# Performance work log

Hardware: AMD Instinct MI355X
Metric: run time of the kernel (lower is better)

## Reference

```python
import jax, jax.numpy as jnp
from jax import lax
import numpy as np

ALPHA = 0.82
MAXITER = 10
N1_NODES = 2048
N2_NODES = 2048
K_ATTR = 64
EDGE_P = 0.004  # sparse-ish adjacency density


def setup_inputs() -> dict:
    key = jax.random.key(0)
    k1, k2, k3, k4 = jax.random.split(key, 4)
    A1 = (jax.random.uniform(k1, (N1_NODES, N1_NODES)) < EDGE_P).astype(jnp.float32)
    A1 = jnp.maximum(A1, A1.T)  # undirected 0/1 adjacency
    A2 = (jax.random.uniform(k2, (N2_NODES, N2_NODES)) < EDGE_P).astype(jnp.float32)
    A2 = jnp.maximum(A2, A2.T)
    N1 = jax.random.uniform(k3, (N1_NODES, K_ATTR), dtype=jnp.float32)
    N2 = jax.random.uniform(k4, (N2_NODES, K_ATTR), dtype=jnp.float32)
    # default prior (_get_H with path=None), normalized so sum ~= 1
    H = jnp.full((N2_NODES, N1_NODES), 1.0 / (N1_NODES * N2_NODES), dtype=jnp.float32)
    return {"A1": A1, "A2": A2, "N1": N1, "N2": N2, "H": H}


def _row_l2_normalize(N):
    nrm = jnp.sqrt(jnp.sum(N * N, axis=1, keepdims=True))
    return jnp.where(nrm > 0, N / jnp.where(nrm > 0, nrm, 1.0), 0.0)


def _final_forward(A1, A2, N1, N2, H, alpha=ALPHA, maxiter=MAXITER):
    # No edge attrs: L=1, E1=A1, E2=A2. T = 1/A^2 where A^2>0 (elementwise),
    # E <- E*T, so B = (E*A) = A*T*A.
    def masked_recip_sq(A):
        A2e = A * A
        return jnp.where(A2e > 0, 1.0 / jnp.where(A2e > 0, A2e, 1.0), 0.0)

    B1 = (A1 * masked_recip_sq(A1)) * A1  # (n1, n1)
    B2 = (A2 * masked_recip_sq(A2)) * A2  # (n2, n2)

    N1n = _row_l2_normalize(N1)  # (n1, K)
    N2n = _row_l2_normalize(N2)  # (n2, K)

    # Kronecker vectors laid out as (n1, n2) matrices (C-order == kron order):
    # N[i*n2+j] = sum_k N1[i,k]*N2[j,k]  -> N1n @ N2n.T
    Nm = N1n @ N2n.T  # (n1, n2)
    dm = (B1 @ N1n) @ (B2 @ N2n).T  # (n1, n2)
    D = Nm * dm
    DD = jnp.where(D > 0, lax.rsqrt(jnp.where(D > 0, D, 1.0)), 0.0)  # inf -> 0
    q = DD * Nm  # (n1, n2)

    # h = H.flatten('F') with H (n2,n1): as an (n1,n2) matrix this is H.T
    h = H.T  # (n1, n2)

    def step(s, _):
        # M = (q*s) reshaped (n2,n1) F-order == (q*s).T in our layout.
        # S = B2 @ M @ B1 (n2,n1); S.flatten('F') as (n1,n2) == B1.T @ (q*s) @ B2.T
        S_t = B1.T @ (q * s) @ B2.T  # (n1, n2)
        s_new = (1.0 - alpha) * h + alpha * q * S_t
        return s_new, None

    s, _ = lax.scan(step, h, None, length=maxiter)
    # original: s.reshape((n1, n2)) C-order -> exactly our layout
    return s  # (n1, n2) alignment matrix


def reference(A1, A2, N1, N2, H):
    return _final_forward(A1, A2, N1, N2, H)
```

## Files before the change

kernel.cpp:

```cpp
#include <hip/hip_runtime.h>

#define NMAT 2048
#define KATTR 64
#define CAP 128
#define NITER 10

typedef unsigned short ushort4v __attribute__((ext_vector_type(4)));

__device__ __forceinline__ unsigned short f2bf(float f) {
  unsigned u = __float_as_uint(f);
  return (unsigned short)((u + 0x7fff + ((u >> 16) & 1)) >> 16);
}
__device__ __forceinline__ float bf2f(unsigned short b) {
  return __uint_as_float((unsigned)b << 16);
}
__device__ __forceinline__ float bflo(unsigned v) {
  return __uint_as_float(v << 16);
}
__device__ __forceinline__ float bfhi(unsigned v) {
  return __uint_as_float(v & 0xffff0000u);
}
__device__ __forceinline__ int swz(int c) { return 4 * c + (((c >> 3) & 7) << 2); }

__global__ __launch_bounds__(256) void k_build(
    const float* __restrict__ A, unsigned short* __restrict__ idx,
    unsigned short* __restrict__ idxT, int* __restrict__ cnt) {
  __shared__ int lcnt;
  int r = blockIdx.x;
  if (threadIdx.x == 0) lcnt = 0;
  __syncthreads();
  const float* row = A + (size_t)r * NMAT;
  for (int c = threadIdx.x; c < NMAT; c += 256) {
    if (row[c] != 0.0f) {
      int p = atomicAdd(&lcnt, 1);
      if (p < CAP) {
        idx[r * CAP + p] = (unsigned short)c;
        if (idxT) idxT[(size_t)p * NMAT + r] = (unsigned short)c;
      }
    }
  }
  __syncthreads();
  if (threadIdx.x == 0) cnt[r] = lcnt < CAP ? lcnt : CAP;
}

__global__ __launch_bounds__(256) void k_norm(const float* __restrict__ Nin,
                                              float* __restrict__ Nout) {
  int row = blockIdx.x * 4 + (threadIdx.x >> 6);
  int lane = threadIdx.x & 63;
  float v = Nin[(size_t)row * KATTR + lane];
  float ss = v * v;
#pragma unroll
  for (int o = 32; o > 0; o >>= 1) ss += __shfl_xor(ss, o);
  float nrm = sqrtf(ss);
  Nout[(size_t)row * KATTR + lane] = (nrm > 0.f) ? v / nrm : 0.f;
}

__global__ void k_gatherN(const unsigned short* __restrict__ idx,
                          const int* __restrict__ cnt,
                          const float* __restrict__ Nn,
                          float* __restrict__ C) {
  int i = blockIdx.x;
  int lane = threadIdx.x;
  int nn = cnt[i];
  const unsigned short* ip = idx + i * CAP;
  float acc = 0.f;
  for (int t = 0; t < nn; ++t) {
    int k = ip[t];
    acc += Nn[(size_t)k * KATTR + lane];
  }
  C[(size_t)i * KATTR + lane] = acc;
}

__global__ __launch_bounds__(256) void k_transpose(const float* __restrict__ H,
                                                   float* __restrict__ Ht) {
  __shared__ float tile[64][65];
  int j0 = blockIdx.x * 64;
  int i0 = blockIdx.y * 64;
  int c = threadIdx.x & 63;
  int r0 = threadIdx.x >> 6;
  for (int r = r0; r < 64; r += 4)
    tile[r][c] = H[(size_t)(j0 + r) * NMAT + i0 + c];
  __syncthreads();
  for (int r = r0; r < 64; r += 4)
    Ht[(size_t)(i0 + r) * NMAT + j0 + c] = tile[c][r];
}

__global__ __launch_bounds__(256) void k_q(
    const float* __restrict__ N1n, const float* __restrict__ C1,
    const float* __restrict__ N2n, const float* __restrict__ C2,
    const float* __restrict__ Ht, float* __restrict__ q,
    float* __restrict__ Q2, unsigned short* __restrict__ M,
    unsigned short* __restrict__ M0base) {
  __shared__ float sA[64][68];
  __shared__ float sB[64][68];
  int i0 = blockIdx.y * 64, j0 = blockIdx.x * 64;
  int c = threadIdx.x & 63, r0 = threadIdx.x >> 6;
  int tx = threadIdx.x & 15, ty = threadIdx.x >> 4;
  const float alpha = 0.82f;

  float nmv[4][4] = {};
  float dmv[4][4] = {};

  for (int r = r0; r < 64; r += 4) {
    sA[c][r] = N1n[(size_t)(i0 + r) * KATTR + c];
    sB[c][r] = N2n[(size_t)(j0 + r) * KATTR + c];
  }
  __syncthreads();
#pragma unroll 4
  for (int k = 0; k < 64; ++k) {
    float4 a = *(const float4*)&sA[k][ty * 4];
    float4 b = *(const float4*)&sB[k][tx * 4];
    float av[4] = {a.x, a.y, a.z, a.w};
    float bv[4] = {b.x, b.y, b.z, b.w};
#pragma unroll
    for (int ii = 0; ii < 4; ++ii)
#pragma unroll
      for (int jj = 0; jj < 4; ++jj)
        nmv[ii][jj] = fmaf(av[ii], bv[jj], nmv[ii][jj]);
  }
  __syncthreads();
  for (int r = r0; r < 64; r += 4) {
    sA[c][r] = C1[(size_t)(i0 + r) * KATTR + c];
    sB[c][r] = C2[(size_t)(j0 + r) * KATTR + c];
  }
  __syncthreads();
#pragma unroll 4
  for (int k = 0; k < 64; ++k) {
    float4 a = *(const float4*)&sA[k][ty * 4];
    float4 b = *(const float4*)&sB[k][tx * 4];
    float av[4] = {a.x, a.y, a.z, a.w};
    float bv[4] = {b.x, b.y, b.z, b.w};
#pragma unroll
    for (int ii = 0; ii < 4; ++ii)
#pragma unroll
      for (int jj = 0; jj < 4; ++jj)
        dmv[ii][jj] = fmaf(av[ii], bv[jj], dmv[ii][jj]);
  }

#pragma unroll
  for (int ii = 0; ii < 4; ++ii) {
    int i = i0 + ty * 4 + ii;
    size_t base = (size_t)i * NMAT + j0 + tx * 4;
    float4 hv = *(const float4*)&Ht[base];
    float hvv[4] = {hv.x, hv.y, hv.z, hv.w};
    float qv[4], q2v[4];
    ushort4v mv, m0v;
#pragma unroll
    for (int jj = 0; jj < 4; ++jj) {
      float nmx = nmv[ii][jj];
      float D = nmx * dmv[ii][jj];
      float qq = (D > 0.f) ? nmx * rsqrtf(D) : 0.f;
      qv[jj] = qq;
      q2v[jj] = alpha * qq * qq;
      float m0 = qq * hvv[jj];
      mv[jj] = f2bf(m0);
      m0v[jj] = f2bf((1.0f - alpha) * m0);
    }
    *(float4*)&q[base] = make_float4(qv[0], qv[1], qv[2], qv[3]);
    *(float4*)&Q2[base] = make_float4(q2v[0], q2v[1], q2v[2], q2v[3]);
    *(ushort4v*)&M[base] = mv;
    *(ushort4v*)&M0base[base] = m0v;
  }
}

__global__ __launch_bounds__(1024, 8) void k_iter(
    const unsigned short* __restrict__ idx1, const int* __restrict__ cnt1,
    const unsigned short* __restrict__ idx2T, const int* __restrict__ cnt2,
    const unsigned short* __restrict__ Min, const float* __restrict__ MinF,
    const float* __restrict__ Q2, const unsigned short* __restrict__ M0base,
    const float* __restrict__ q, const float* __restrict__ Ht,
    unsigned short* __restrict__ Mout, float* __restrict__ MoutF,
    float* __restrict__ sout, int in32, int out32, int last) {
  __shared__ float lds[4 * NMAT + 32];
  int i0 = blockIdx.x * 4;
  int tid = threadIdx.x;
  int c0 = tid * 2;

  float acc[4][2];
#pragma unroll
  for (int r = 0; r < 4; ++r) {
    int nn = cnt1[i0 + r];
    const unsigned short* ip = idx1 + (i0 + r) * CAP;
    float a0 = 0.f, a1 = 0.f;
    float b0 = 0.f, b1 = 0.f;
    if (in32) {
      int t = 0;
      for (; t + 4 <= nn; t += 4) {
        uint2 pk = *(const uint2*)(ip + t);
        int k0 = pk.x & 0xffff, k1 = pk.x >> 16;
        int k2 = pk.y & 0xffff, k3 = pk.y >> 16;
        float2 v0 = *(const float2*)(MinF + (size_t)k0 * NMAT + c0);
        float2 v1 = *(const float2*)(MinF + (size_t)k1 * NMAT + c0);
        float2 v2 = *(const float2*)(MinF + (size_t)k2 * NMAT + c0);
        float2 v3 = *(const float2*)(MinF + (size_t)k3 * NMAT + c0);
        a0 += v0.x + v1.x; a1 += v0.y + v1.y;
        b0 += v2.x + v3.x; b1 += v2.y + v3.y;
      }
      for (; t < nn; ++t) {
        float2 v0 = *(const float2*)(MinF + (size_t)ip[t] * NMAT + c0);
        a0 += v0.x; a1 += v0.y;
      }
    } else {
      int t = 0;
      for (; t + 8 <= nn; t += 8) {
        uint4 pk = *(const uint4*)(ip + t);
        int k0 = pk.x & 0xffff, k1 = pk.x >> 16;
        int k2 = pk.y & 0xffff, k3 = pk.y >> 16;
        int k4 = pk.z & 0xffff, k5 = pk.z >> 16;
        int k6 = pk.w & 0xffff, k7 = pk.w >> 16;
        unsigned v0 = *(const unsigned*)(Min + (size_t)k0 * NMAT + c0);
        unsigned v1 = *(const unsigned*)(Min + (size_t)k1 * NMAT + c0);
        unsigned v2 = *(const unsigned*)(Min + (size_t)k2 * NMAT + c0);
        unsigned v3 = *(const unsigned*)(Min + (size_t)k3 * NMAT + c0);
        unsigned v4 = *(const unsigned*)(Min + (size_t)k4 * NMAT + c0);
        unsigned v5 = *(const unsigned*)(Min + (size_t)k5 * NMAT + c0);
        unsigned v6 = *(const unsigned*)(Min + (size_t)k6 * NMAT + c0);
        unsigned v7 = *(const unsigned*)(Min + (size_t)k7 * NMAT + c0);
        a0 += bflo(v0) + bflo(v1) + bflo(v2) + bflo(v3);
        a1 += bfhi(v0) + bfhi(v1) + bfhi(v2) + bfhi(v3);
        b0 += bflo(v4) + bflo(v5) + bflo(v6) + bflo(v7);
        b1 += bfhi(v4) + bfhi(v5) + bfhi(v6) + bfhi(v7);
      }
      for (; t + 4 <= nn; t += 4) {
        uint2 pk = *(const uint2*)(ip + t);
        int k0 = pk.x & 0xffff, k1 = pk.x >> 16;
        int k2 = pk.y & 0xffff, k3 = pk.y >> 16;
        unsigned v0 = *(const unsigned*)(Min + (size_t)k0 * NMAT + c0);
        unsigned v1 = *(const unsigned*)(Min + (size_t)k1 * NMAT + c0);
        unsigned v2 = *(const unsigned*)(Min + (size_t)k2 * NMAT + c0);
        unsigned v3 = *(const unsigned*)(Min + (size_t)k3 * NMAT + c0);
        a0 += bflo(v0) + bflo(v1) + bflo(v2) + bflo(v3);
        a1 += bfhi(v0) + bfhi(v1) + bfhi(v2) + bfhi(v3);
      }
      for (; t < nn; ++t) {
        unsigned v0 = *(const unsigned*)(Min + (size_t)ip[t] * NMAT + c0);
        a0 += bflo(v0); a1 += bfhi(v0);
      }
    }
    acc[r][0] = a0 + b0;
    acc[r][1] = a1 + b1;
  }
  *(float4*)&lds[swz(c0)] =
      make_float4(acc[0][0], acc[1][0], acc[2][0], acc[3][0]);
  *(float4*)&lds[swz(c0 + 1)] =
      make_float4(acc[0][1], acc[1][1], acc[2][1], acc[3][1]);
  __syncthreads();

  const float alpha = 0.82f;
  const float oma = 1.0f - alpha;
#pragma unroll
  for (int jj = 0; jj < 2; ++jj) {
    int j = jj * 1024 + tid;
    int nn = cnt2[j];
    const unsigned short* ip = idx2T + j;
    float s0 = 0.f, s1 = 0.f, s2 = 0.f, s3 = 0.f;
    float u0 = 0.f, u1 = 0.f, u2 = 0.f, u3 = 0.f;
    int t = 0;
    for (; t + 4 <= nn; t += 4) {
      int ka = ip[(size_t)t * NMAT];
      int kb = ip[(size_t)(t + 1) * NMAT];
      int kc = ip[(size_t)(t + 2) * NMAT];
      int kd = ip[(size_t)(t + 3) * NMAT];
      float4 va = *(const float4*)&lds[swz(ka)];
      float4 vb = *(const float4*)&lds[swz(kb)];
      float4 vc = *(const float4*)&lds[swz(kc)];
      float4 vd = *(const float4*)&lds[swz(kd)];
      s0 += va.x + vc.x; s1 += va.y + vc.y;
      s2 += va.z + vc.z; s3 += va.w + vc.w;
      u0 += vb.x + vd.x; u1 += vb.y + vd.y;
      u2 += vb.z + vd.z; u3 += vb.w + vd.w;
    }
    for (; t < nn; ++t) {
      int ka = ip[(size_t)t * NMAT];
      float4 va = *(const float4*)&lds[swz(ka)];
      s0 += va.x; s1 += va.y; s2 += va.z; s3 += va.w;
    }
    float sa[4] = {s0 + u0, s1 + u1, s2 + u2, s3 + u3};
    if (last) {
#pragma unroll
      for (int r = 0; r < 4; ++r) {
        size_t off = (size_t)(i0 + r) * NMAT + j;
        sout[off] = oma * Ht[off] + alpha * q[off] * sa[r];
      }
    } else if (out32) {
#pragma unroll
      for (int r = 0; r < 4; ++r) {
        size_t off = (size_t)(i0 + r) * NMAT + j;
        MoutF[off] = fmaf(Q2[off], sa[r], bf2f(M0base[off]));
      }
    } else {
#pragma unroll
      for (int r = 0; r < 4; ++r) {
        size_t off = (size_t)(i0 + r) * NMAT + j;
        Mout[off] = f2bf(fmaf(Q2[off], sa[r], bf2f(M0base[off])));
      }
    }
  }
}

extern "C" void kernel_launch(void* const* d_in, const int* in_sizes, int n_in,
                              void* d_out, int out_size, void* d_ws,
                              size_t ws_size, hipStream_t stream) {
  const float* A1 = (const float*)d_in[0];
  const float* A2 = (const float*)d_in[1];
  const float* N1 = (const float*)d_in[2];
  const float* N2 = (const float*)d_in[3];
  const float* H = (const float*)d_in[4];
  float* s_out = (float*)d_out;

  char* p = (char*)d_ws;
  auto take = [&](size_t bytes) {
    char* r = p;
    p += (bytes + 255) & ~(size_t)255;
    return r;
  };
  unsigned short* idx1 = (unsigned short*)take((size_t)NMAT * CAP * 2);
  unsigned short* idx2 = (unsigned short*)take((size_t)NMAT * CAP * 2);
  unsigned short* idx2T = (unsigned short*)take((size_t)CAP * NMAT * 2);
  int* cnt1 = (int*)take((size_t)NMAT * 4);
  int* cnt2 = (int*)take((size_t)NMAT * 4);
  float* N1n = (float*)take((size_t)NMAT * KATTR * 4);
  float* N2n = (float*)take((size_t)NMAT * KATTR * 4);
  float* C1 = (float*)take((size_t)NMAT * KATTR * 4);
  float* C2 = (float*)take((size_t)NMAT * KATTR * 4);
  float* Ht = (float*)take((size_t)NMAT * NMAT * 4);
  float* q = (float*)take((size_t)NMAT * NMAT * 4);
  float* Q2 = (float*)take((size_t)NMAT * NMAT * 4);
  unsigned short* Mb0 = (unsigned short*)take((size_t)NMAT * NMAT * 2);
  unsigned short* Mb1 = (unsigned short*)take((size_t)NMAT * NMAT * 2);
  unsigned short* M0b = (unsigned short*)take((size_t)NMAT * NMAT * 2);
  float* Mf = (float*)take((size_t)NMAT * NMAT * 4);
  if ((size_t)(p - (char*)d_ws) > ws_size) return;

  k_build<<<NMAT, 256, 0, stream>>>(A1, idx1, (unsigned short*)nullptr, cnt1);
  k_build<<<NMAT, 256, 0, stream>>>(A2, idx2, idx2T, cnt2);
  k_norm<<<NMAT / 4, 256, 0, stream>>>(N1, N1n);
  k_norm<<<NMAT / 4, 256, 0, stream>>>(N2, N2n);
  k_gatherN<<<NMAT, 64, 0, stream>>>(idx1, cnt1, N1n, C1);
  k_gatherN<<<NMAT, 64, 0, stream>>>(idx2, cnt2, N2n, C2);
  k_transpose<<<dim3(32, 32), 256, 0, stream>>>(H, Ht);
  k_q<<<dim3(32, 32), 256, 0, stream>>>(N1n, C1, N2n, C2, Ht, q, Q2, Mb0,
                                        M0b);
  for (int it = 0; it < NITER; ++it) {
    const unsigned short* Min = (it & 1) ? Mb1 : Mb0;
    unsigned short* Mout = (it & 1) ? Mb0 : Mb1;
    int in32 = (it == NITER - 1) ? 1 : 0;
    int out32 = (it == NITER - 2) ? 1 : 0;
    int last = (it == NITER - 1) ? 1 : 0;
    k_iter<<<NMAT / 4, 1024, 0, stream>>>(idx1, cnt1, idx2T, cnt2, Min, Mf,
                                          Q2, M0b, q, Ht, Mout, Mf, s_out,
                                          in32, out32, last);
  }
}
```

Baseline: 458.3 us.

## Split iteration into stripe-blocked LDS gather and second-side gather kernels

Each of the first nine iterations is split into two kernels. The first stores the bf16 iterate in a 16-column stripe-blocked layout so each block can stage a whole 2048x16 stripe in LDS and do the B1 gather from shared memory instead of scattered global loads. The second reads the intermediate T1 in fp32 and performs the B2 gather and update, writing back in the blocked layout. This costs an extra fp32 intermediate round trip through global memory and one extra launch per iteration. The final iteration keeps the fused fp32 kernel.

New measurement: 474.2 us. +3.5%, slower.

```diff
diff --git a/kernel.cpp b/kernel.cpp
--- a/kernel.cpp
+++ b/kernel.cpp
@@ -4,6 +4,8 @@
 #define KATTR 64
 #define CAP 128
 #define NITER 10
+#define NSTRIPE 128
+#define LSTRIDE 9
 
 typedef unsigned short ushort4v __attribute__((ext_vector_type(4)));
 
@@ -21,6 +23,9 @@
   return __uint_as_float(v & 0xffff0000u);
 }
 __device__ __forceinline__ int swz(int c) { return 4 * c + (((c >> 3) & 7) << 2); }
+__device__ __forceinline__ size_t bidx(int i, int j) {
+  return ((size_t)(j >> 4) * NMAT + i) * 16 + (j & 15);
+}
 
 __global__ __launch_bounds__(256) void k_build(
     const float* __restrict__ A, unsigned short* __restrict__ idx,
@@ -89,7 +94,7 @@
     const float* __restrict__ N1n, const float* __restrict__ C1,
     const float* __restrict__ N2n, const float* __restrict__ C2,
     const float* __restrict__ Ht, float* __restrict__ q,
-    float* __restrict__ Q2, unsigned short* __restrict__ M,
+    float* __restrict__ Q2, unsigned short* __restrict__ Mblk,
     unsigned short* __restrict__ M0base) {
   __shared__ float sA[64][68];
   __shared__ float sB[64][68];
@@ -140,7 +145,8 @@
 #pragma unroll
   for (int ii = 0; ii < 4; ++ii) {
     int i = i0 + ty * 4 + ii;
-    size_t base = (size_t)i * NMAT + j0 + tx * 4;
+    int jb = j0 + tx * 4;
+    size_t base = (size_t)i * NMAT + jb;
     float4 hv = *(const float4*)&Ht[base];
     float hvv[4] = {hv.x, hv.y, hv.z, hv.w};
     float qv[4], q2v[4];
@@ -158,96 +164,80 @@
     }
     *(float4*)&q[base] = make_float4(qv[0], qv[1], qv[2], qv[3]);
     *(float4*)&Q2[base] = make_float4(q2v[0], q2v[1], q2v[2], q2v[3]);
-    *(ushort4v*)&M[base] = mv;
+    *(ushort4v*)&Mblk[bidx(i, jb)] = mv;
     *(ushort4v*)&M0base[base] = m0v;
   }
 }
 
-__global__ __launch_bounds__(1024, 8) void k_iter(
+__global__ __launch_bounds__(1024, 8) void k1s(
     const unsigned short* __restrict__ idx1, const int* __restrict__ cnt1,
+    const unsigned short* __restrict__ Mblk, float* __restrict__ T1) {
+  __shared__ unsigned lds[NMAT * LSTRIDE];
+  int stripe = blockIdx.x & (NSTRIPE - 1);
+  int chunk = blockIdx.x >> 7;
+  int tid = threadIdx.x;
+  const unsigned* src = (const unsigned*)(Mblk + (size_t)stripe * NMAT * 16);
+#pragma unroll
+  for (int p = 0; p < 4; ++p) {
+    int e = p * 4096 + tid * 4;
+    uint4 v = *(const uint4*)(src + e);
+    int row = e >> 3;
+    int cc = e & 7;
+    lds[row * LSTRIDE + cc] = v.x;
+    lds[row * LSTRIDE + cc + 1] = v.y;
+    lds[row * LSTRIDE + cc + 2] = v.z;
+    lds[row * LSTRIDE + cc + 3] = v.w;
+  }
+  __syncthreads();
+
+  int i = chunk * 512 + (tid >> 1);
+  int h = tid & 1;
+  int nn = cnt1[i];
+  const unsigned short* ip = idx1 + i * CAP;
+  float a0 = 0, a1 = 0, a2 = 0, a3 = 0, a4 = 0, a5 = 0, a6 = 0, a7 = 0;
+  int t = 0;
+  for (; t + 2 <= nn; t += 2) {
+    unsigned pr = *(const unsigned*)(ip + t);
+    int ka = (int)(pr & 0xffff) * LSTRIDE + h * 4;
+    int kb = (int)(pr >> 16) * LSTRIDE + h * 4;
+    unsigned w0 = lds[ka], w1 = lds[ka + 1], w2 = lds[ka + 2], w3 = lds[ka + 3];
+    unsigned x0 = lds[kb], x1 = lds[kb + 1], x2 = lds[kb + 2], x3 = lds[kb + 3];
+    a0 += bflo(w0) + bflo(x0); a1 += bfhi(w0) + bfhi(x0);
+    a2 += bflo(w1) + bflo(x1); a3 += bfhi(w1) + bfhi(x1);
+    a4 += bflo(w2) + bflo(x2); a5 += bfhi(w2) + bfhi(x2);
+    a6 += bflo(w3) + bflo(x3); a7 += bfhi(w3) + bfhi(x3);
+  }
+  if (t < nn) {
+    int ka = (int)ip[t] * LSTRIDE + h * 4;
+    unsigned w0 = lds[ka], w1 = lds[ka + 1], w2 = lds[ka + 2], w3 = lds[ka + 3];
+    a0 += bflo(w0); a1 += bfhi(w0);
+    a2 += bflo(w1); a3 += bfhi(w1);
+    a4 += bflo(w2); a5 += bfhi(w2);
+    a6 += bflo(w3); a7 += bfhi(w3);
+  }
+  float* dst = T1 + (size_t)i * NMAT + stripe * 16 + h * 8;
+  *(float4*)dst = make_float4(a0, a1, a2, a3);
+  *(float4*)(dst + 4) = make_float4(a4, a5, a6, a7);
+}
+
+__global__ __launch_bounds__(1024, 8) void k2s(
     const unsigned short* __restrict__ idx2T, const int* __restrict__ cnt2,
-    const unsigned short* __restrict__ Min, const float* __restrict__ MinF,
-    const float* __restrict__ Q2, const unsigned short* __restrict__ M0base,
-    const float* __restrict__ q, const float* __restrict__ Ht,
-    unsigned short* __restrict__ Mout, float* __restrict__ MoutF,
-    float* __restrict__ sout, int in32, int out32, int last) {
+    const float* __restrict__ T1, const float* __restrict__ Q2,
+    const unsigned short* __restrict__ M0base,
+    unsigned short* __restrict__ Moutb, float* __restrict__ MoutF,
+    int out32) {
   __shared__ float lds[4 * NMAT + 32];
   int i0 = blockIdx.x * 4;
   int tid = threadIdx.x;
   int c0 = tid * 2;
-
-  float acc[4][2];
-#pragma unroll
-  for (int r = 0; r < 4; ++r) {
-    int nn = cnt1[i0 + r];
-    const unsigned short* ip = idx1 + (i0 + r) * CAP;
-    float a0 = 0.f, a1 = 0.f;
-    float b0 = 0.f, b1 = 0.f;
-    if (in32) {
-      int t = 0;
-      for (; t + 4 <= nn; t += 4) {
-        uint2 pk = *(const uint2*)(ip + t);
-        int k0 = pk.x & 0xffff, k1 = pk.x >> 16;
-        int k2 = pk.y & 0xffff, k3 = pk.y >> 16;
-        float2 v0 = *(const float2*)(MinF + (size_t)k0 * NMAT + c0);
-        float2 v1 = *(const float2*)(MinF + (size_t)k1 * NMAT + c0);
-        float2 v2 = *(const float2*)(MinF + (size_t)k2 * NMAT + c0);
-        float2 v3 = *(const float2*)(MinF + (size_t)k3 * NMAT + c0);
-        a0 += v0.x + v1.x; a1 += v0.y + v1.y;
-        b0 += v2.x + v3.x; b1 += v2.y + v3.y;
-      }
-      for (; t < nn; ++t) {
-        float2 v0 = *(const float2*)(MinF + (size_t)ip[t] * NMAT + c0);
-        a0 += v0.x; a1 += v0.y;
-      }
-    } else {
-      int t = 0;
-      for (; t + 8 <= nn; t += 8) {
-        uint4 pk = *(const uint4*)(ip + t);
-        int k0 = pk.x & 0xffff, k1 = pk.x >> 16;
-        int k2 = pk.y & 0xffff, k3 = pk.y >> 16;
-        int k4 = pk.z & 0xffff, k5 = pk.z >> 16;
-        int k6 = pk.w & 0xffff, k7 = pk.w >> 16;
-        unsigned v0 = *(const unsigned*)(Min + (size_t)k0 * NMAT + c0);
-        unsigned v1 = *(const unsigned*)(Min + (size_t)k1 * NMAT + c0);
-        unsigned v2 = *(const unsigned*)(Min + (size_t)k2 * NMAT + c0);
-        unsigned v3 = *(const unsigned*)(Min + (size_t)k3 * NMAT + c0);
-        unsigned v4 = *(const unsigned*)(Min + (size_t)k4 * NMAT + c0);
-        unsigned v5 = *(const unsigned*)(Min + (size_t)k5 * NMAT + c0);
-        unsigned v6 = *(const unsigned*)(Min + (size_t)k6 * NMAT + c0);
-        unsigned v7 = *(const unsigned*)(Min + (size_t)k7 * NMAT + c0);
-        a0 += bflo(v0) + bflo(v1) + bflo(v2) + bflo(v3);
-        a1 += bfhi(v0) + bfhi(v1) + bfhi(v2) + bfhi(v3);
-        b0 += bflo(v4) + bflo(v5) + bflo(v6) + bflo(v7);
-        b1 += bfhi(v4) + bfhi(v5) + bfhi(v6) + bfhi(v7);
-      }
-      for (; t + 4 <= nn; t += 4) {
-        uint2 pk = *(const uint2*)(ip + t);
-        int k0 = pk.x & 0xffff, k1 = pk.x >> 16;
-        int k2 = pk.y & 0xffff, k3 = pk.y >> 16;
-        unsigned v0 = *(const unsigned*)(Min + (size_t)k0 * NMAT + c0);
-        unsigned v1 = *(const unsigned*)(Min + (size_t)k1 * NMAT + c0);
-        unsigned v2 = *(const unsigned*)(Min + (size_t)k2 * NMAT + c0);
-        unsigned v3 = *(const unsigned*)(Min + (size_t)k3 * NMAT + c0);
-        a0 += bflo(v0) + bflo(v1) + bflo(v2) + bflo(v3);
-        a1 += bfhi(v0) + bfhi(v1) + bfhi(v2) + bfhi(v3);
-      }
-      for (; t < nn; ++t) {
-        unsigned v0 = *(const unsigned*)(Min + (size_t)ip[t] * NMAT + c0);
-        a0 += bflo(v0); a1 += bfhi(v0);
-      }
-    }
-    acc[r][0] = a0 + b0;
-    acc[r][1] = a1 + b1;
-  }
-  *(float4*)&lds[swz(c0)] =
-      make_float4(acc[0][0], acc[1][0], acc[2][0], acc[3][0]);
-  *(float4*)&lds[swz(c0 + 1)] =
-      make_float4(acc[0][1], acc[1][1], acc[2][1], acc[3][1]);
-  __syncthreads();
-
-  const float alpha = 0.82f;
-  const float oma = 1.0f - alpha;
+  float2 v[4];
+#pragma unroll
+  for (int r = 0; r < 4; ++r)
+    v[r] = *(const float2*)(T1 + (size_t)(i0 + r) * NMAT + c0);
+  *(float4*)&lds[swz(c0)] = make_float4(v[0].x, v[1].x, v[2].x, v[3].x);
+  *(float4*)&lds[swz(c0 + 1)] = make_float4(v[0].y, v[1].y, v[2].y, v[3].y);
+  __syncthreads();
+
 #pragma unroll
   for (int jj = 0; jj < 2; ++jj) {
     int j = jj * 1024 + tid;
@@ -276,13 +266,7 @@
       s0 += va.x; s1 += va.y; s2 += va.z; s3 += va.w;
     }
     float sa[4] = {s0 + u0, s1 + u1, s2 + u2, s3 + u3};
-    if (last) {
-#pragma unroll
-      for (int r = 0; r < 4; ++r) {
-        size_t off = (size_t)(i0 + r) * NMAT + j;
-        sout[off] = oma * Ht[off] + alpha * q[off] * sa[r];
-      }
-    } else if (out32) {
+    if (out32) {
 #pragma unroll
       for (int r = 0; r < 4; ++r) {
         size_t off = (size_t)(i0 + r) * NMAT + j;
@@ -292,8 +276,88 @@
 #pragma unroll
       for (int r = 0; r < 4; ++r) {
         size_t off = (size_t)(i0 + r) * NMAT + j;
-        Mout[off] = f2bf(fmaf(Q2[off], sa[r], bf2f(M0base[off])));
+        Moutb[bidx(i0 + r, j)] = f2bf(fmaf(Q2[off], sa[r], bf2f(M0base[off])));
       }
+    }
+  }
+}
+
+__global__ __launch_bounds__(1024, 8) void k_iter(
+    const unsigned short* __restrict__ idx1, const int* __restrict__ cnt1,
+    const unsigned short* __restrict__ idx2T, const int* __restrict__ cnt2,
+    const float* __restrict__ MinF, const float* __restrict__ q,
+    const float* __restrict__ Ht, float* __restrict__ sout) {
+  __shared__ float lds[4 * NMAT + 32];
+  int i0 = blockIdx.x * 4;
+  int tid = threadIdx.x;
+  int c0 = tid * 2;
+
+  float acc[4][2];
+#pragma unroll
+  for (int r = 0; r < 4; ++r) {
+    int nn = cnt1[i0 + r];
+    const unsigned short* ip = idx1 + (i0 + r) * CAP;
+    float a0 = 0.f, a1 = 0.f;
+    float b0 = 0.f, b1 = 0.f;
+    int t = 0;
+    for (; t + 4 <= nn; t += 4) {
+      uint2 pk = *(const uint2*)(ip + t);
+      int k0 = pk.x & 0xffff, k1 = pk.x >> 16;
+      int k2 = pk.y & 0xffff, k3 = pk.y >> 16;
+      float2 v0 = *(const float2*)(MinF + (size_t)k0 * NMAT + c0);
+      float2 v1 = *(const float2*)(MinF + (size_t)k1 * NMAT + c0);
+      float2 v2 = *(const float2*)(MinF + (size_t)k2 * NMAT + c0);
+      float2 v3 = *(const float2*)(MinF + (size_t)k3 * NMAT + c0);
+      a0 += v0.x + v1.x; a1 += v0.y + v1.y;
+      b0 += v2.x + v3.x; b1 += v2.y + v3.y;
+    }
+    for (; t < nn; ++t) {
+      float2 v0 = *(const float2*)(MinF + (size_t)ip[t] * NMAT + c0);
+      a0 += v0.x; a1 += v0.y;
+    }
+    acc[r][0] = a0 + b0;
+    acc[r][1] = a1 + b1;
+  }
+  *(float4*)&lds[swz(c0)] =
+      make_float4(acc[0][0], acc[1][0], acc[2][0], acc[3][0]);
+  *(float4*)&lds[swz(c0 + 1)] =
+      make_float4(acc[0][1], acc[1][1], acc[2][1], acc[3][1]);
+  __syncthreads();
+
+  const float alpha = 0.82f;
+  const float oma = 1.0f - alpha;
+#pragma unroll
+  for (int jj = 0; jj < 2; ++jj) {
+    int j = jj * 1024 + tid;
+    int nn = cnt2[j];
+    const unsigned short* ip = idx2T + j;
+    float s0 = 0.f, s1 = 0.f, s2 = 0.f, s3 = 0.f;
+    float u0 = 0.f, u1 = 0.f, u2 = 0.f, u3 = 0.f;
+    int t = 0;
+    for (; t + 4 <= nn; t += 4) {
+      int ka = ip[(size_t)t * NMAT];
+      int kb = ip[(size_t)(t + 1) * NMAT];
+      int kc = ip[(size_t)(t + 2) * NMAT];
+      int kd = ip[(size_t)(t + 3) * NMAT];
+      float4 va = *(const float4*)&lds[swz(ka)];
+      float4 vb = *(const float4*)&lds[swz(kb)];
+      float4 vc = *(const float4*)&lds[swz(kc)];
+      float4 vd = *(const float4*)&lds[swz(kd)];
+      s0 += va.x + vc.x; s1 += va.y + vc.y;
+      s2 += va.z + vc.z; s3 += va.w + vc.w;
+      u0 += vb.x + vd.x; u1 += vb.y + vd.y;
+      u2 += vb.z + vd.z; u3 += vb.w + vd.w;
+    }
+    for (; t < nn; ++t) {
+      int ka = ip[(size_t)t * NMAT];
+      float4 va = *(const float4*)&lds[swz(ka)];
+      s0 += va.x; s1 += va.y; s2 += va.z; s3 += va.w;
+    }
+    float sa[4] = {s0 + u0, s1 + u1, s2 + u2, s3 + u3};
+#pragma unroll
+    for (int r = 0; r < 4; ++r) {
+      size_t off = (size_t)(i0 + r) * NMAT + j;
+      sout[off] = oma * Ht[off] + alpha * q[off] * sa[r];
     }
   }
 }
@@ -330,6 +394,7 @@
   unsigned short* Mb1 = (unsigned short*)take((size_t)NMAT * NMAT * 2);
   unsigned short* M0b = (unsigned short*)take((size_t)NMAT * NMAT * 2);
   float* Mf = (float*)take((size_t)NMAT * NMAT * 4);
+  float* T1 = (float*)take((size_t)NMAT * NMAT * 4);
   if ((size_t)(p - (char*)d_ws) > ws_size) return;
 
   k_build<<<NMAT, 256, 0, stream>>>(A1, idx1, (unsigned short*)nullptr, cnt1);
@@ -341,14 +406,14 @@
   k_transpose<<<dim3(32, 32), 256, 0, stream>>>(H, Ht);
   k_q<<<dim3(32, 32), 256, 0, stream>>>(N1n, C1, N2n, C2, Ht, q, Q2, Mb0,
                                         M0b);
-  for (int it = 0; it < NITER; ++it) {
+  for (int it = 0; it < NITER - 1; ++it) {
     const unsigned short* Min = (it & 1) ? Mb1 : Mb0;
     unsigned short* Mout = (it & 1) ? Mb0 : Mb1;
-    int in32 = (it == NITER - 1) ? 1 : 0;
     int out32 = (it == NITER - 2) ? 1 : 0;
-    int last = (it == NITER - 1) ? 1 : 0;
-    k_iter<<<NMAT / 4, 1024, 0, stream>>>(idx1, cnt1, idx2T, cnt2, Min, Mf,
-                                          Q2, M0b, q, Ht, Mout, Mf, s_out,
-                                          in32, out32, last);
-  }
-}
+    k1s<<<4 * NSTRIPE, 1024, 0, stream>>>(idx1, cnt1, Min, T1);
+    k2s<<<NMAT / 4, 1024, 0, stream>>>(idx2T, cnt2, T1, Q2, M0b, Mout, Mf,
+                                       out32);
+  }
+  k_iter<<<NMAT / 4, 1024, 0, stream>>>(idx1, cnt1, idx2T, cnt2, Mf, q, Ht,
+                                        s_out);
+}
```
